# Kernel optimization log

Hardware: AMD Instinct MI355X
Metric: run time of the kernel (lower is better)

Reference implementation:

```python
import jax, jax.numpy as jnp
import numpy as np

N, C, D = 8192, 6, 512


def setup_inputs() -> dict:
    key = jax.random.key(0)
    k1, k2, k3, k4 = jax.random.split(key, 4)
    logits = jax.random.normal(k1, (N, C), dtype=jnp.float32)      # unused by the loss
    targets = jax.random.uniform(k2, (N, C), dtype=jnp.float32)    # soft labels
    features = jax.random.normal(k3, (N, D), dtype=jnp.float32)
    weights = jax.random.uniform(k4, (N,), dtype=jnp.float32)
    t = jnp.asarray(10.0, dtype=jnp.float32)   # nn.Parameter init
    b = jnp.asarray(-10.0, dtype=jnp.float32)  # nn.Parameter init
    return {"logits": logits, "targets": targets, "features": features,
            "weights": weights, "t": t, "b": b}


def reference(logits, targets, features, weights, t, b):
    # F.normalize(features, p=2, dim=1) with eps=1e-12 clamp like torch
    norm = jnp.maximum(jnp.linalg.norm(features, axis=1, keepdims=True), 1e-12)
    f = features / norm                                   # [N, D]
    sim = jnp.einsum('nd,md->nm', f, f)                   # [N, N] cosine similarity
    agree = 2.0 * jnp.einsum('nc,mc->nm', targets, targets) - 1.0  # [N, N]
    elements = agree * (t * sim + b)
    # -log(1/(1+exp(e))) == softplus(e) == -log_sigmoid(-e), numerically stable
    loss = (1.0 / N) * (-jax.nn.log_sigmoid(-elements)).sum(axis=1)  # [N]
    loss = loss * weights / weights.mean()
    return loss
```

## Files before the change

### kernel.cpp

```cpp
#include <hip/hip_runtime.h>
#include <hip/hip_bf16.h>


#define NROW 8192
#define DIM  512
#define NCLS 6

#define BM 128
#define BK 64
#define NB (NROW / BM)
#define NTRI (NB * (NB + 1) / 2)
#define NSTG 8

typedef short s16x8 __attribute__((ext_vector_type(8)));
typedef float f32x4 __attribute__((ext_vector_type(4)));

static __device__ __forceinline__ ushort f2bf(float x) {
    __hip_bfloat16 h = __float2bfloat16(x);
    union { __hip_bfloat16 h; ushort u; } c; c.h = h; return c.u;
}

__global__ __launch_bounds__(256) void k_prep(const float* __restrict__ feat,
                                              const float* __restrict__ w,
                                              ushort* __restrict__ fpack,
                                              float* __restrict__ partial,
                                              float* __restrict__ wpart) {
    const int wave = threadIdx.x >> 6, lane = threadIdx.x & 63;
    const int row = blockIdx.x * 4 + wave;
    const float* fr = feat + (size_t)row * DIM;
    float4 v0 = *(const float4*)(fr + lane * 4);
    float4 v1 = *(const float4*)(fr + 256 + lane * 4);
    float ss = v0.x*v0.x + v0.y*v0.y + v0.z*v0.z + v0.w*v0.w
             + v1.x*v1.x + v1.y*v1.y + v1.z*v1.z + v1.w*v1.w;
#pragma unroll
    for (int m = 1; m < 64; m <<= 1) ss += __shfl_xor(ss, m);
    const float inv = 1.f / fmaxf(sqrtf(ss), 1e-12f);

    float vals[8] = {v0.x, v0.y, v0.z, v0.w, v1.x, v1.y, v1.z, v1.w};
    ushort hi[8];
#pragma unroll
    for (int i = 0; i < 8; ++i) hi[i] = f2bf(vals[i] * inv);
    ushort* dst = fpack + (size_t)row * 512;
    *(ushort4*)(dst + lane * 4)       = make_ushort4(hi[0], hi[1], hi[2], hi[3]);
    *(ushort4*)(dst + 256 + lane * 4) = make_ushort4(hi[4], hi[5], hi[6], hi[7]);

    __shared__ float red[4];
    if (lane == 0) {
        partial[row] = 0.f;
        red[wave] = w[row];
    }
    __syncthreads();
    if (threadIdx.x == 0)
        wpart[blockIdx.x] = red[0] + red[1] + red[2] + red[3];
}

__device__ __forceinline__ void stage_f(const ushort* __restrict__ src,
                                        ushort* lds, int tid) {
#pragma unroll
    for (int i = 0; i < 4; ++i) {
        int q = i * 256 + tid;
        int r = q >> 3, c = q & 7;
        __builtin_amdgcn_global_load_lds(
            (const __attribute__((address_space(1))) void*)(src + (size_t)r * 512 + c * 8),
            (__attribute__((address_space(3))) void*)(lds + q * 8),
            16, 0, 0);
    }
}

__global__ __launch_bounds__(256, 3) void k_gemm(
    const ushort* __restrict__ fpack, const float* __restrict__ tgt,
    const float* __restrict__ tp, const float* __restrict__ bp,
    float* __restrict__ partial) {

    const int orig = blockIdx.x;
    const int b = (orig & 7) * (NTRI / 8) + (orig >> 3);
    int bi = 0, rem = b;
    while (rem >= NB - bi) { rem -= NB - bi; ++bi; }
    const int bj = bi + rem;

    __shared__ ushort sA[BM * BK];
    __shared__ ushort sB[BM * BK];

    const int tid = threadIdx.x;
    const int lane = tid & 63;
    const int wave = tid >> 6;
    const int wr = wave >> 1, wc = wave & 1;

    const float tt = *tp, bb = *bp;

    f32x4 acc[4][4];
#pragma unroll
    for (int i = 0; i < 4; ++i)
#pragma unroll
        for (int j = 0; j < 4; ++j)
            acc[i][j] = (f32x4){0.f, 0.f, 0.f, 0.f};

    const ushort* baseA = fpack + (size_t)(bi * BM) * 512;
    const ushort* baseB = fpack + (size_t)(bj * BM) * 512;

    for (int s = 0; s < NSTG; ++s) {
        stage_f(baseA + s * 64, &sA[0], tid);
        stage_f(baseB + s * 64, &sB[0], tid);
        __syncthreads();
#pragma unroll
        for (int kk = 0; kk < 2; ++kk) {
            s16x8 af[4], bg[4];
            const int kb = kk * 32 + (lane >> 4) * 8;
            const int rr = lane & 15;
#pragma unroll
            for (int i = 0; i < 4; ++i)
                af[i] = *(const s16x8*)(&sA[(wr * 64 + i * 16 + rr) * BK + kb]);
#pragma unroll
            for (int j = 0; j < 4; ++j)
                bg[j] = *(const s16x8*)(&sB[(wc * 64 + j * 16 + rr) * BK + kb]);
#pragma unroll
            for (int i = 0; i < 4; ++i)
#pragma unroll
                for (int j = 0; j < 4; ++j)
                    acc[i][j] = __builtin_amdgcn_mfma_f32_16x16x32_bf16(
                        af[i], bg[j], acc[i][j], 0, 0, 0);
        }
        __syncthreads();
    }

    float* sTA = (float*)&sA[0];
    float* sTB = (float*)&sB[0];
    for (int q = tid; q < BM * NCLS; q += 256) {
        sTA[q] = tgt[(size_t)(bi * BM) * NCLS + q];
        sTB[q] = tgt[(size_t)(bj * BM) * NCLS + q];
    }
    __syncthreads();

    float tcol[4][NCLS];
#pragma unroll
    for (int j = 0; j < 4; ++j) {
        const int col = wc * 64 + j * 16 + (lane & 15);
#pragma unroll
        for (int c = 0; c < NCLS; ++c) tcol[j][c] = sTB[col * NCLS + c];
    }

    float rowsum[4][4];
    float colsum[4];
#pragma unroll
    for (int i = 0; i < 4; ++i)
#pragma unroll
        for (int r = 0; r < 4; ++r) rowsum[i][r] = 0.f;
#pragma unroll
    for (int j = 0; j < 4; ++j) colsum[j] = 0.f;

#pragma unroll
    for (int i = 0; i < 4; ++i)
#pragma unroll
        for (int r = 0; r < 4; ++r) {
            const int row = wr * 64 + i * 16 + (lane >> 4) * 4 + r;
            float trow[NCLS];
#pragma unroll
            for (int c = 0; c < NCLS; ++c) trow[c] = sTA[row * NCLS + c];
#pragma unroll
            for (int j = 0; j < 4; ++j) {
                float d = 0.f;
#pragma unroll
                for (int c = 0; c < NCLS; ++c) d = fmaf(trow[c], tcol[j][c], d);
                const float agree = fmaf(2.f, d, -1.f);
                const float e = agree * fmaf(tt, acc[i][j][r], bb);
                float sp;
                if (__all(e < -6.f)) {
                    const float x = __expf(e);
                    sp = x * fmaf(-0.5f, x, 1.f);
                } else {
                    sp = fmaxf(e, 0.f) + __logf(1.f + __expf(-fabsf(e)));
                }
                rowsum[i][r] += sp;
                colsum[j] += sp;
            }
        }

#pragma unroll
    for (int i = 0; i < 4; ++i)
#pragma unroll
        for (int r = 0; r < 4; ++r) {
            float v = rowsum[i][r];
            v += __shfl_xor(v, 1); v += __shfl_xor(v, 2);
            v += __shfl_xor(v, 4); v += __shfl_xor(v, 8);
            if ((lane & 15) == 0)
                atomicAdd(&partial[bi * BM + wr * 64 + i * 16 + (lane >> 4) * 4 + r], v);
        }
    if (bi != bj) {
#pragma unroll
        for (int j = 0; j < 4; ++j) {
            float v = colsum[j];
            v += __shfl_xor(v, 16); v += __shfl_xor(v, 32);
            if (lane < 16)
                atomicAdd(&partial[bj * BM + wc * 64 + j * 16 + lane], v);
        }
    }
}

__global__ __launch_bounds__(256) void k_final(const float* __restrict__ partial,
                                               const float* __restrict__ w,
                                               const float* __restrict__ wpart,
                                               float* __restrict__ out) {
    __shared__ float red[4];
    float s = 0.f;
    for (int i = threadIdx.x; i < NROW / 4; i += 256) s += wpart[i];
#pragma unroll
    for (int m = 1; m < 64; m <<= 1) s += __shfl_xor(s, m);
    if ((threadIdx.x & 63) == 0) red[threadIdx.x >> 6] = s;
    __syncthreads();
    const float wsum = red[0] + red[1] + red[2] + red[3];
    int i = blockIdx.x * 256 + threadIdx.x;
    out[i] = partial[i] * w[i] / wsum;
}

extern "C" void kernel_launch(void* const* d_in, const int* in_sizes, int n_in,
                              void* d_out, int out_size, void* d_ws, size_t ws_size,
                              hipStream_t stream) {
    const float* targets  = (const float*)d_in[1];
    const float* features = (const float*)d_in[2];
    const float* weights  = (const float*)d_in[3];
    const float* tp       = (const float*)d_in[4];
    const float* bp       = (const float*)d_in[5];
    float* out = (float*)d_out;

    char* p = (char*)d_ws;
    ushort* fpack   = (ushort*)p; p += (size_t)NROW * 512 * sizeof(ushort);
    float*  partial = (float*)p;  p += (size_t)NROW * sizeof(float);
    float*  wpart   = (float*)p;  p += (size_t)(NROW / 4) * sizeof(float);

    k_prep<<<NROW / 4, 256, 0, stream>>>(features, weights, fpack, partial, wpart);
    k_gemm<<<NTRI, 256, 0, stream>>>(fpack, targets, tp, bp, partial);
    k_final<<<NROW / 256, 256, 0, stream>>>(partial, weights, wpart, out);
}
```

Baseline: 174.4 us.

## Swizzle packed features to avoid LDS bank conflicts, supertile block order, raise occupancy

The prep kernel now writes each row's bf16 features with an XOR swizzle of 8-element chunks keyed on row%8, and the GEMM reads LDS with the matching XOR so fragment loads avoid bank conflicts. The triangular block index is remapped into 8x8 supertiles to improve L2 reuse of A/B panels. Launch bounds go from 3 to 4 blocks per CU, which may limit registers and cause spills. The wave-uniform small-e fast path for softplus is dropped in favour of a single branch-free formula.

After: 209.7 us. 1.2x slower.

```diff
diff --git a/kernel.cpp b/kernel.cpp
--- a/kernel.cpp
+++ b/kernel.cpp
@@ -41,8 +41,9 @@
 #pragma unroll
     for (int i = 0; i < 8; ++i) hi[i] = f2bf(vals[i] * inv);
     ushort* dst = fpack + (size_t)row * 512;
-    *(ushort4*)(dst + lane * 4)       = make_ushort4(hi[0], hi[1], hi[2], hi[3]);
-    *(ushort4*)(dst + 256 + lane * 4) = make_ushort4(hi[4], hi[5], hi[6], hi[7]);
+    const int sw = (row & 7) << 3;
+    *(ushort4*)(dst + ((lane * 4) ^ sw))       = make_ushort4(hi[0], hi[1], hi[2], hi[3]);
+    *(ushort4*)(dst + ((256 + lane * 4) ^ sw)) = make_ushort4(hi[4], hi[5], hi[6], hi[7]);
 
     __shared__ float red[4];
     if (lane == 0) {
@@ -67,16 +68,28 @@
     }
 }
 
-__global__ __launch_bounds__(256, 3) void k_gemm(
+__global__ __launch_bounds__(256, 4) void k_gemm(
     const ushort* __restrict__ fpack, const float* __restrict__ tgt,
     const float* __restrict__ tp, const float* __restrict__ bp,
     float* __restrict__ partial) {
 
     const int orig = blockIdx.x;
-    const int b = (orig & 7) * (NTRI / 8) + (orig >> 3);
-    int bi = 0, rem = b;
-    while (rem >= NB - bi) { rem -= NB - bi; ++bi; }
-    const int bj = bi + rem;
+    int b = (orig & 7) * (NTRI / 8) + (orig >> 3);
+    int SI = 0, rem = b;
+    while (rem >= 36 + (7 - SI) * 64) { rem -= 36 + (7 - SI) * 64; ++SI; }
+    int bi, bj;
+    if (rem < 36) {
+        int ii = 0;
+        while (rem >= 8 - ii) { rem -= 8 - ii; ++ii; }
+        bi = SI * 8 + ii;
+        bj = SI * 8 + ii + rem;
+    } else {
+        const int r2 = rem - 36;
+        const int SJ = SI + 1 + (r2 >> 6);
+        const int idx = r2 & 63;
+        bi = SI * 8 + (idx >> 3);
+        bj = SJ * 8 + (idx & 7);
+    }
 
     __shared__ ushort sA[BM * BK];
     __shared__ ushort sB[BM * BK];
@@ -97,6 +110,8 @@
 
     const ushort* baseA = fpack + (size_t)(bi * BM) * 512;
     const ushort* baseB = fpack + (size_t)(bj * BM) * 512;
+    const int rr = lane & 15;
+    const int ksw = (lane & 7) << 3;
 
     for (int s = 0; s < NSTG; ++s) {
         stage_f(baseA + s * 64, &sA[0], tid);
@@ -105,8 +120,7 @@
 #pragma unroll
         for (int kk = 0; kk < 2; ++kk) {
             s16x8 af[4], bg[4];
-            const int kb = kk * 32 + (lane >> 4) * 8;
-            const int rr = lane & 15;
+            const int kb = (kk * 32 + (lane >> 4) * 8) ^ ksw;
 #pragma unroll
             for (int i = 0; i < 4; ++i)
                 af[i] = *(const s16x8*)(&sA[(wr * 64 + i * 16 + rr) * BK + kb]);
@@ -163,13 +177,7 @@
                 for (int c = 0; c < NCLS; ++c) d = fmaf(trow[c], tcol[j][c], d);
                 const float agree = fmaf(2.f, d, -1.f);
                 const float e = agree * fmaf(tt, acc[i][j][r], bb);
-                float sp;
-                if (__all(e < -6.f)) {
-                    const float x = __expf(e);
-                    sp = x * fmaf(-0.5f, x, 1.f);
-                } else {
-                    sp = fmaxf(e, 0.f) + __logf(1.f + __expf(-fabsf(e)));
-                }
+                const float sp = fmaxf(e, 0.f) + __logf(1.f + __expf(-fabsf(e)));
                 rowsum[i][r] += sp;
                 colsum[j] += sp;
             }
```
